# Kernel tuning notes

Measured on AMD Instinct MI355X. Metric: run time of the kernel, lower is better.

## Reference

```python
import jax, jax.numpy as jnp
import numpy as np

B, NQ, ISIZE = 8, 2048, 1024
H, D, NA = 8, 128, 8            # num_head, attn_dim, num_anchor
AH = H * D                      # ahsize = 1024
ASZ = NA * D                    # anchor_size = 1024
FH = 4096                       # _fhsize
ISZ_NET = FH * H // NA          # 4096, input dim of self.net
EPS = 1e-6


def setup_inputs() -> dict:
    key = jax.random.key(0)
    ks = jax.random.split(key, 12)
    def u(k, shape, fan_in):
        s = 1.0 / np.sqrt(fan_in)
        return jax.random.uniform(k, shape, jnp.float32, -s, s)
    return {
        "inputs": jax.random.normal(ks[0], (B, NQ, ISIZE), jnp.float32),
        "ln_g": jnp.ones((ISIZE,), jnp.float32),
        "ln_b": jnp.zeros((ISIZE,), jnp.float32),
        "q_anchor": u(ks[1], (H, NA, D), D),
        "W_qkv": u(ks[2], (ISIZE, 3 * AH), ISIZE), "b_qkv": jnp.zeros((3 * AH,), jnp.float32),
        "W_an": u(ks[3], (ASZ, FH), ASZ), "b_an": jnp.zeros((FH,), jnp.float32),
        "W_n1": u(ks[4], (ISZ_NET, AH), ISZ_NET), "b_n1": jnp.zeros((AH,), jnp.float32),
        "W_n2": u(ks[5], (AH, FH), AH), "b_n2": jnp.zeros((FH,), jnp.float32),
        "W_n3": u(ks[6], (FH, AH), FH), "b_n3": jnp.zeros((AH,), jnp.float32),
        "W_k": u(ks[7], (AH, AH), AH), "b_k": jnp.zeros((AH,), jnp.float32),
        "W_o": u(ks[8], (AH, ISIZE), AH), "b_o": jnp.zeros((ISIZE,), jnp.float32),
    }


def reference(inputs, ln_g, ln_b, q_anchor, W_qkv, b_qkv, W_an, b_an,
              W_n1, b_n1, W_n2, b_n2, W_n3, b_n3, W_k, b_k, W_o, b_o):
    b, nq = inputs.shape[:2]
    scale = 1.0 / np.sqrt(D)
    # pre-LayerNorm
    mu = jnp.mean(inputs, -1, keepdims=True)
    var = jnp.mean(jnp.square(inputs - mu), -1, keepdims=True)
    x = (inputs - mu) * jax.lax.rsqrt(var + EPS) * ln_g + ln_b
    # QKV projection
    qkv = (x @ W_qkv + b_qkv).reshape(b, nq, 3, H, D)
    q = jnp.transpose(qkv[:, :, 0], (0, 2, 1, 3))   # [b,H,nq,D]
    k = qkv[:, :, 1]                                  # [b,nq,H,D]
    v = qkv[:, :, 2]                                  # [b,nq,H,D]
    # stage 1: fixed anchors attend over the sequence
    sc1 = jax.nn.softmax(jnp.einsum('had,bnhd->bhan', q_anchor, k) * scale, axis=-1)
    out = jnp.einsum('bhan,bnhd->bhad', sc1, v).reshape(b, H, ASZ)   # [b,H,NA*D]
    # anchor_net (share_head Linear + ReLU)
    out = jax.nn.relu(out @ W_an + b_an)                              # [b,H,FH]
    # regroup head-major -> anchor-major
    out = out.reshape(b, H, NA, FH // NA).transpose(0, 2, 1, 3).reshape(b, NA, ISZ_NET)
    # net: bottleneck Linear -> Linear -> ReLU -> Linear
    out = jax.nn.relu((out @ W_n1 + b_n1) @ W_n2 + b_n2) @ W_n3 + b_n3  # [b,NA,AH]
    # stage 2: queries attend over anchors
    kk = (out @ W_k + b_k).reshape(b, NA, H, D)
    sc2 = jax.nn.softmax(jnp.einsum('bhqd,bahd->bhqa', q, kk) * scale, axis=-1)
    ov = out.reshape(b, NA, H, D)
    y = jnp.einsum('bhqa,bahd->bqhd', sc2, ov).reshape(b, nq, AH)
    return y @ W_o + b_o + inputs
```

## Files before the change

### kernel.cpp

```cpp
#include <hip/hip_runtime.h>
#include <cstdint>
#include <cstddef>

typedef unsigned short u16;
typedef __attribute__((ext_vector_type(8))) short short8;
typedef __attribute__((ext_vector_type(4))) float floatx4;
typedef __attribute__((ext_vector_type(16))) float floatx16;

__device__ __forceinline__ u16 f2bf(float f) {
  unsigned u = __float_as_uint(f);
  u += 0x7fffu + ((u >> 16) & 1u);
  return (u16)(u >> 16);
}
__device__ __forceinline__ float bf2f(u16 s) {
  return __uint_as_float(((unsigned)s) << 16);
}

__global__ __launch_bounds__(256) void ln_kernel(const float* __restrict__ x,
                                                 const float* __restrict__ g,
                                                 const float* __restrict__ bta,
                                                 u16* __restrict__ out) {
  const int row = blockIdx.x;
  const int tid = threadIdx.x;
  const float4 v = ((const float4*)(x + (size_t)row * 1024))[tid];
  float s = v.x + v.y + v.z + v.w;
#pragma unroll
  for (int o = 32; o > 0; o >>= 1) s += __shfl_down(s, o);
  __shared__ float red[4], red2[4];
  const int wv = tid >> 6, ln = tid & 63;
  if (ln == 0) red[wv] = s;
  __syncthreads();
  const float mean = (red[0] + red[1] + red[2] + red[3]) * (1.0f / 1024.0f);
  const float dx = v.x - mean, dy = v.y - mean, dz = v.z - mean, dw = v.w - mean;
  float s2 = dx * dx + dy * dy + dz * dz + dw * dw;
#pragma unroll
  for (int o = 32; o > 0; o >>= 1) s2 += __shfl_down(s2, o);
  if (ln == 0) red2[wv] = s2;
  __syncthreads();
  const float var = (red2[0] + red2[1] + red2[2] + red2[3]) * (1.0f / 1024.0f);
  const float rstd = rsqrtf(var + 1e-6f);
  const float4 gg = ((const float4*)g)[tid];
  const float4 bb = ((const float4*)bta)[tid];
  ushort4 o4;
  o4.x = f2bf(dx * rstd * gg.x + bb.x);
  o4.y = f2bf(dy * rstd * gg.y + bb.y);
  o4.z = f2bf(dz * rstd * gg.z + bb.z);
  o4.w = f2bf(dw * rstd * gg.w + bb.w);
  ((ushort4*)(out + (size_t)row * 1024))[tid] = o4;
}

__global__ __launch_bounds__(256) void transpose_bf16(const float* __restrict__ W,
                                                      u16* __restrict__ WT,
                                                      int K, int N) {
  __shared__ float t[32][33];
  const int kb = blockIdx.x * 32, nb = blockIdx.y * 32;
  const int tx = threadIdx.x & 31, ty = threadIdx.x >> 5;
#pragma unroll
  for (int i = ty; i < 32; i += 8) t[i][tx] = W[(size_t)(kb + i) * N + nb + tx];
  __syncthreads();
#pragma unroll
  for (int i = ty; i < 32; i += 8) WT[(size_t)(nb + i) * K + kb + tx] = f2bf(t[tx][i]);
}


__device__ __forceinline__ void stageG(const u16* __restrict__ gp, u16* lp, int K) {
  __builtin_amdgcn_global_load_lds((const __attribute__((address_space(1))) void*)gp,
                                   (__attribute__((address_space(3))) void*)lp, 16, 0, 0);
  __builtin_amdgcn_global_load_lds((const __attribute__((address_space(1))) void*)(gp + ((size_t)K << 6)),
                                   (__attribute__((address_space(3))) void*)(lp + 4096), 16, 0, 0);
}

__device__ __forceinline__ void rdA(short8 (&af)[2][4], const u16* sbuf, const int (&ab)[4],
                                    int halfoff) {
#pragma unroll
  for (int mi = 0; mi < 2; ++mi)
#pragma unroll
    for (int ks = 0; ks < 4; ++ks)
      af[mi][ks] = *(const short8*)(sbuf + halfoff + mi * 2048 + (ab[ks] ^ (mi << 5)));
}
__device__ __forceinline__ void rdB(short8 (&bf)[4], const u16* sbuf, const int (&bb)[4],
                                    int halfoff) {
#pragma unroll
  for (int ks = 0; ks < 4; ++ks)
    bf[ks] = *(const short8*)(sbuf + halfoff + bb[ks]);
}

template <int Q>
__device__ __forceinline__ void mfmaQ(floatx16 (&acc)[4][2], const short8 (&af)[2][4],
                                      const short8 (&bf)[4]) {
#pragma unroll
  for (int ks = 0; ks < 4; ++ks)
#pragma unroll
    for (int mi = 0; mi < 2; ++mi)
      acc[Q][mi] = __builtin_amdgcn_mfma_f32_32x32x16_bf16(af[mi][ks], bf[ks], acc[Q][mi], 0, 0, 0);
}

template <int B_>
__device__ __forceinline__ void gtile(int t, int NT, int K,
                                      u16 (&sA)[2][16384], u16 (&sB)[2][16384],
                                      const u16* gA_lo, const u16* gA_hi,
                                      const u16* gB_lo, const u16* gB_hi,
                                      u16* ldsA_cur, u16* ldsA_alt,
                                      u16* ldsB_cur, u16* ldsB_alt,
                                      const int (&ab)[4], const int (&bb)[4],
                                      floatx16 (&acc)[4][2],
                                      short8 (&afA)[2][4], short8 (&bfP)[4], short8 (&bfN)[4]) {
  rdA(afA, sA[B_], ab, 0);
  __builtin_amdgcn_sched_barrier(0);
  if (t + 1 < NT) stageG(gA_hi + ((t + 1) << 6), ldsA_alt + 8192, K);
  rdB(bfN, sB[B_], bb, 8192);
  asm volatile("s_waitcnt lgkmcnt(4)" ::: "memory");
  __builtin_amdgcn_sched_barrier(0);
  __builtin_amdgcn_s_setprio(1);
  mfmaQ<0>(acc, afA, bfP);
  __builtin_amdgcn_s_setprio(0);
  if (t + 1 < NT) stageG(gB_lo + ((t + 1) << 6), ldsB_alt, K);
  asm volatile("s_waitcnt lgkmcnt(0)" ::: "memory");
  __builtin_amdgcn_sched_barrier(0);
  __builtin_amdgcn_s_setprio(1);
  mfmaQ<1>(acc, afA, bfN);
  __builtin_amdgcn_s_setprio(0);
  rdA(afA, sA[B_], ab, 8192);
  __builtin_amdgcn_s_barrier();
  if (t + 2 < NT) stageG(gA_lo + ((t + 2) << 6), ldsA_cur, K);
  asm volatile("s_waitcnt lgkmcnt(0)" ::: "memory");
  __builtin_amdgcn_sched_barrier(0);
  __builtin_amdgcn_s_setprio(1);
  mfmaQ<2>(acc, afA, bfN);
  __builtin_amdgcn_s_setprio(0);
  if (t + 2 < NT) stageG(gB_hi + ((t + 2) << 6), ldsB_cur + 8192, K);
  if (t + 2 < NT) {
    asm volatile("s_waitcnt vmcnt(4)" ::: "memory");
  } else {
    asm volatile("s_waitcnt vmcnt(0)" ::: "memory");
  }
  __builtin_amdgcn_s_barrier();
  if (t + 1 < NT) rdB(bfN, sB[B_ ^ 1], bb, 0);
  __builtin_amdgcn_sched_barrier(0);
  __builtin_amdgcn_s_setprio(1);
  mfmaQ<3>(acc, afA, bfP);
  __builtin_amdgcn_s_setprio(0);
}

template <int EPI>
__global__ __launch_bounds__(512, 2) void gemm_bf16(const u16* __restrict__ A,
                                                    const u16* __restrict__ BT,
                                                    const float* __restrict__ bias,
                                                    const float* __restrict__ extra,
                                                    u16* __restrict__ outB,
                                                    float* __restrict__ outF,
                                                    int M, int N, int K) {
  __shared__ u16 sA[2][16384];
  __shared__ u16 sB[2][16384];
  const int tid = threadIdx.x;
  const int wave = tid >> 6, lane = tid & 63;
  const int m0 = blockIdx.x * 256, n0 = blockIdx.y * 256;
  const int wr = wave >> 2, wc = wave & 3;
  const int l31 = lane & 31, l5 = lane >> 5, l7 = lane & 7;
  const int NT = K >> 6;

  const int fa = l7 ^ (l31 >> 3);
  const int fb = l7 ^ ((wc * 4 + (l31 >> 3)) & 7);
  int ab[4], bb[4];
#pragma unroll
  for (int ks = 0; ks < 4; ++ks) {
    const int kg = (ks << 1) + l5;
    ab[ks] = (wr * 64 + l31) * 64 + (((kg ^ fa) & 7) << 3);
    bb[ks] = (wc * 32 + l31) * 64 + (((kg ^ fb) & 7) << 3);
  }
  const int srow = wave * 8 + (lane >> 3);
  const int scol = ((lane & 7) ^ (lane >> 3) ^ wave) << 3;
  const u16* gA_lo = A + (size_t)(m0 + srow) * K + scol;
  const u16* gA_hi = A + (size_t)(m0 + 128 + srow) * K + scol;
  const u16* gB_lo = BT + (size_t)(n0 + srow) * K + scol;
  const u16* gB_hi = BT + (size_t)(n0 + 128 + srow) * K + scol;

  floatx16 acc[4][2];
#pragma unroll
  for (int q = 0; q < 4; ++q)
#pragma unroll
    for (int mi = 0; mi < 2; ++mi)
#pragma unroll
      for (int r = 0; r < 16; ++r) acc[q][mi][r] = 0.f;

  stageG(gA_lo, &sA[0][0] + wave * 512, K);
  stageG(gA_hi, &sA[0][8192] + wave * 512, K);
  stageG(gB_lo, &sB[0][0] + wave * 512, K);
  stageG(gB_hi, &sB[0][8192] + wave * 512, K);
  stageG(gA_lo + 64, &sA[1][0] + wave * 512, K);
  stageG(gB_hi + 64, &sB[1][8192] + wave * 512, K);
  asm volatile("s_waitcnt vmcnt(4)" ::: "memory");
  __builtin_amdgcn_s_barrier();

  short8 afA[2][4], bfX[4], bfY[4];
  rdB(bfX, sB[0], bb, 0);
  __builtin_amdgcn_sched_barrier(0);

  for (int t = 0; t < NT; t += 2) {
    gtile<0>(t, NT, K, sA, sB, gA_lo, gA_hi, gB_lo, gB_hi,
             &sA[0][0] + wave * 512, &sA[1][0] + wave * 512,
             &sB[0][0] + wave * 512, &sB[1][0] + wave * 512, ab, bb, acc, afA, bfX, bfY);
    gtile<1>(t + 1, NT, K, sA, sB, gA_lo, gA_hi, gB_lo, gB_hi,
             &sA[1][0] + wave * 512, &sA[0][0] + wave * 512,
             &sB[1][0] + wave * 512, &sB[0][0] + wave * 512, ab, bb, acc, afA, bfY, bfX);
  }

#pragma unroll
  for (int q = 0; q < 4; ++q) {
    const int QM = q >> 1, QN = QM ^ (q & 1);
    const int n = n0 + QN * 128 + wc * 32 + l31;
    const float bs = bias[n];
#pragma unroll
    for (int mi = 0; mi < 2; ++mi) {
      const int mb = m0 + QM * 128 + wr * 64 + mi * 32 + 4 * l5;
#pragma unroll
      for (int reg = 0; reg < 16; ++reg) {
        const int m = mb + (reg & 3) + 8 * (reg >> 2);
        const float v = acc[q][mi][reg] + bs;
        if (EPI == 0)
          outB[(size_t)m * N + n] = f2bf(v);
        else
          outF[(size_t)m * N + n] = v + extra[(size_t)m * N + n];
      }
    }
  }
}

__global__ __launch_bounds__(256) void attn1_scores(const u16* __restrict__ qkv,
                                                    const float* __restrict__ q_anchor,
                                                    float* __restrict__ S) {
  __shared__ float qa[8][128];
  const int tid = threadIdx.x;
  const int chunk = blockIdx.x & 7, bh = blockIdx.x >> 3;
  const int b = bh >> 3, h = bh & 7;
  for (int i = tid; i < 1024; i += 256) qa[i >> 7][i & 127] = q_anchor[h * 1024 + i];
  __syncthreads();
  const float scale = 0.0883883476483184f;
  const int n = chunk * 256 + tid;
  const u16* kp = qkv + (size_t)(b * 2048 + n) * 3072 + 1024 + h * 128;
  float dots[8] = {0, 0, 0, 0, 0, 0, 0, 0};
#pragma unroll 8
  for (int dd = 0; dd < 128; dd += 4) {
    const ushort4 k4 = *(const ushort4*)(kp + dd);
    const float k0 = bf2f(k4.x), k1 = bf2f(k4.y), k2 = bf2f(k4.z), k3 = bf2f(k4.w);
#pragma unroll
    for (int a = 0; a < 8; ++a) {
      const float4 q4 = *(const float4*)&qa[a][dd];
      dots[a] += q4.x * k0 + q4.y * k1 + q4.z * k2 + q4.w * k3;
    }
  }
#pragma unroll
  for (int a = 0; a < 8; ++a) S[((size_t)(bh * 8 + a)) * 2048 + n] = dots[a] * scale;
}

__global__ __launch_bounds__(256) void attn1_softmax(float* __restrict__ S) {
  const int row = blockIdx.x;
  const int tid = threadIdx.x;
  float* Sp = S + (size_t)row * 2048;
  float4 v0 = ((const float4*)Sp)[tid * 2];
  float4 v1 = ((const float4*)Sp)[tid * 2 + 1];
  float mx = fmaxf(fmaxf(fmaxf(v0.x, v0.y), fmaxf(v0.z, v0.w)),
                   fmaxf(fmaxf(v1.x, v1.y), fmaxf(v1.z, v1.w)));
#pragma unroll
  for (int o = 32; o > 0; o >>= 1) mx = fmaxf(mx, __shfl_xor(mx, o));
  __shared__ float red[4];
  const int wv = tid >> 6, ln = tid & 63;
  if (ln == 0) red[wv] = mx;
  __syncthreads();
  mx = fmaxf(fmaxf(red[0], red[1]), fmaxf(red[2], red[3]));
  v0.x = __expf(v0.x - mx); v0.y = __expf(v0.y - mx);
  v0.z = __expf(v0.z - mx); v0.w = __expf(v0.w - mx);
  v1.x = __expf(v1.x - mx); v1.y = __expf(v1.y - mx);
  v1.z = __expf(v1.z - mx); v1.w = __expf(v1.w - mx);
  float sum = v0.x + v0.y + v0.z + v0.w + v1.x + v1.y + v1.z + v1.w;
#pragma unroll
  for (int o = 32; o > 0; o >>= 1) sum += __shfl_xor(sum, o);
  __shared__ float red2[4];
  if (ln == 0) red2[wv] = sum;
  __syncthreads();
  const float inv = 1.f / (red2[0] + red2[1] + red2[2] + red2[3]);
  v0.x *= inv; v0.y *= inv; v0.z *= inv; v0.w *= inv;
  v1.x *= inv; v1.y *= inv; v1.z *= inv; v1.w *= inv;
  ((float4*)Sp)[tid * 2] = v0;
  ((float4*)Sp)[tid * 2 + 1] = v1;
}

__global__ __launch_bounds__(256) void attn1_pv(const u16* __restrict__ qkv,
                                                const float* __restrict__ S,
                                                float* __restrict__ pvpart) {
  __shared__ float P[8][256];
  const int tid = threadIdx.x;
  const int chunk = blockIdx.x & 7, bh = blockIdx.x >> 3;
  const int b = bh >> 3, h = bh & 7;
  for (int i = tid; i < 2048; i += 256) {
    const int a = i >> 8, n = i & 255;
    P[a][n] = S[((size_t)(bh * 8 + a)) * 2048 + chunk * 256 + n];
  }
  __syncthreads();
  const int d = tid & 127, half = tid >> 7;
  const int nbase = chunk * 256 + half * 128;
  const u16* vp = qkv + (size_t)(b * 2048 + nbase) * 3072 + 2048 + h * 128 + d;
  float acc[8] = {0.f};
  for (int n = 0; n < 128; n += 4) {
    const float v0 = bf2f(vp[(size_t)n * 3072]);
    const float v1 = bf2f(vp[(size_t)(n + 1) * 3072]);
    const float v2 = bf2f(vp[(size_t)(n + 2) * 3072]);
    const float v3 = bf2f(vp[(size_t)(n + 3) * 3072]);
#pragma unroll
    for (int a = 0; a < 8; ++a) {
      const float4 s4 = *(const float4*)&P[a][half * 128 + n];
      acc[a] += s4.x * v0 + s4.y * v1 + s4.z * v2 + s4.w * v3;
    }
  }
  const int split = chunk * 2 + half;
#pragma unroll
  for (int a = 0; a < 8; ++a)
    pvpart[((size_t)split * 64 + bh) * 1024 + a * 128 + d] = acc[a];
}

__global__ __launch_bounds__(256) void mlp_mfma(const float* __restrict__ A,
                                                const float* __restrict__ W,
                                                float* __restrict__ part,
                                                int K, int N, int KC) {
  __shared__ float sW[64][33];
  const int tid = threadIdx.x;
  const int lane = tid & 63, wave = tid >> 6;
  const int wm = wave * 16;
  const int n0 = blockIdx.x * 64;
  const int kbeg = blockIdx.y * KC;
  const int l15 = lane & 15, kq8 = (lane >> 4) * 8;
  const int arow = wm + l15;

  floatx4 acc[4];
  const floatx4 zero = {0.f, 0.f, 0.f, 0.f};
#pragma unroll
  for (int j = 0; j < 4; ++j) acc[j] = zero;

  for (int kc = 0; kc < KC; kc += 32) {
    const int kbase = kbeg + kc;
    __syncthreads();
#pragma unroll
    for (int p = 0; p < 8; ++p) {
      const int k = p * 4 + wave;
      sW[lane][k] = W[(size_t)(kbase + k) * N + n0 + lane];
    }
    const float* ap = A + (size_t)arow * K + kbase + kq8;
    const float4 a0 = *(const float4*)ap;
    const float4 a1 = *(const float4*)(ap + 4);
    short8 af;
    af[0] = (short)f2bf(a0.x); af[1] = (short)f2bf(a0.y);
    af[2] = (short)f2bf(a0.z); af[3] = (short)f2bf(a0.w);
    af[4] = (short)f2bf(a1.x); af[5] = (short)f2bf(a1.y);
    af[6] = (short)f2bf(a1.z); af[7] = (short)f2bf(a1.w);
    __syncthreads();
#pragma unroll
    for (int j = 0; j < 4; ++j) {
      const float* wp = &sW[j * 16 + l15][kq8];
      short8 bf;
      bf[0] = (short)f2bf(wp[0]); bf[1] = (short)f2bf(wp[1]);
      bf[2] = (short)f2bf(wp[2]); bf[3] = (short)f2bf(wp[3]);
      bf[4] = (short)f2bf(wp[4]); bf[5] = (short)f2bf(wp[5]);
      bf[6] = (short)f2bf(wp[6]); bf[7] = (short)f2bf(wp[7]);
      acc[j] = __builtin_amdgcn_mfma_f32_16x16x32_bf16(af, bf, acc[j], 0, 0, 0);
    }
  }
  const int q = lane >> 4;
#pragma unroll
  for (int j = 0; j < 4; ++j)
#pragma unroll
    for (int r = 0; r < 4; ++r) {
      const int m = wm + q * 4 + r;
      const int n = n0 + j * 16 + l15;
      part[((size_t)blockIdx.y * 64 + m) * N + n] = acc[j][r];
    }
}

__global__ __launch_bounds__(256) void mlp_reduce(const float* __restrict__ part,
                                                  const float* __restrict__ bias,
                                                  float* __restrict__ out,
                                                  int N, int nsplit, int relu, int perm) {
  const int idx = blockIdx.x * 256 + threadIdx.x;
  const int e = idx * 4;
  if (e >= 64 * N) return;
  const int row = e / N, col = e - row * N;
  float4 acc;
  if (bias) acc = *(const float4*)&bias[col];
  else { acc.x = 0.f; acc.y = 0.f; acc.z = 0.f; acc.w = 0.f; }
  for (int s = 0; s < nsplit; ++s) {
    const float4 p = *(const float4*)&part[((size_t)s * 64 + row) * N + col];
    acc.x += p.x; acc.y += p.y; acc.z += p.z; acc.w += p.w;
  }
  if (relu) {
    acc.x = fmaxf(acc.x, 0.f); acc.y = fmaxf(acc.y, 0.f);
    acc.z = fmaxf(acc.z, 0.f); acc.w = fmaxf(acc.w, 0.f);
  }
  size_t oidx;
  if (!perm) {
    oidx = (size_t)row * N + col;
  } else {
    const int b = row >> 3, h = row & 7;
    oidx = (size_t)(b * 8 + (col >> 9)) * 4096 + h * 512 + (col & 511);
  }
  *(float4*)&out[oidx] = acc;
}

__global__ __launch_bounds__(256) void attn2_kernel(const u16* __restrict__ qkv,
                                                    const float* __restrict__ kk,
                                                    const float* __restrict__ onet,
                                                    u16* __restrict__ y) {
  __shared__ float kkl[8][128];
  __shared__ float ovl[8][128];
  const int tid = threadIdx.x;
  const int chunk = blockIdx.x & 7, bh = blockIdx.x >> 3;
  const int b = bh >> 3, h = bh & 7;
  for (int i = tid; i < 1024; i += 256) {
    const int a = i >> 7, d = i & 127;
    kkl[a][d] = kk[(size_t)(b * 8 + a) * 1024 + h * 128 + d];
    ovl[a][d] = onet[(size_t)(b * 8 + a) * 1024 + h * 128 + d];
  }
  __syncthreads();
  const int n = chunk * 256 + tid;
  const u16* qp = qkv + (size_t)(b * 2048 + n) * 3072 + h * 128;
  float dots[8] = {0, 0, 0, 0, 0, 0, 0, 0};
#pragma unroll 4
  for (int dd = 0; dd < 128; dd += 4) {
    const ushort4 q4 = *(const ushort4*)(qp + dd);
    const float q0 = bf2f(q4.x), q1 = bf2f(q4.y), q2 = bf2f(q4.z), q3 = bf2f(q4.w);
#pragma unroll
    for (int a = 0; a < 8; ++a) {
      const float4 k4 = *(const float4*)&kkl[a][dd];
      dots[a] += k4.x * q0 + k4.y * q1 + k4.z * q2 + k4.w * q3;
    }
  }
  const float scale = 0.0883883476483184f;
  float mx = -1e30f;
#pragma unroll
  for (int a = 0; a < 8; ++a) {
    dots[a] *= scale;
    mx = fmaxf(mx, dots[a]);
  }
  float p[8];
  float sum = 0.f;
#pragma unroll
  for (int a = 0; a < 8; ++a) {
    p[a] = __expf(dots[a] - mx);
    sum += p[a];
  }
  const float inv = 1.f / sum;
#pragma unroll
  for (int a = 0; a < 8; ++a) p[a] *= inv;
  u16* yp = y + (size_t)(b * 2048 + n) * 1024 + h * 128;
#pragma unroll 4
  for (int dd = 0; dd < 128; dd += 4) {
    float a0 = 0, a1 = 0, a2 = 0, a3 = 0;
#pragma unroll
    for (int a = 0; a < 8; ++a) {
      const float4 o4 = *(const float4*)&ovl[a][dd];
      a0 += p[a] * o4.x;
      a1 += p[a] * o4.y;
      a2 += p[a] * o4.z;
      a3 += p[a] * o4.w;
    }
    ushort4 o;
    o.x = f2bf(a0);
    o.y = f2bf(a1);
    o.z = f2bf(a2);
    o.w = f2bf(a3);
    *(ushort4*)(yp + dd) = o;
  }
}

extern "C" void kernel_launch(void* const* d_in, const int* in_sizes, int n_in,
                              void* d_out, int out_size, void* d_ws, size_t ws_size,
                              hipStream_t stream) {
  const float* inputs = (const float*)d_in[0];
  const float* ln_g = (const float*)d_in[1];
  const float* ln_b = (const float*)d_in[2];
  const float* q_anchor = (const float*)d_in[3];
  const float* W_qkv = (const float*)d_in[4];
  const float* b_qkv = (const float*)d_in[5];
  const float* W_an = (const float*)d_in[6];
  const float* b_an = (const float*)d_in[7];
  const float* W_n1 = (const float*)d_in[8];
  const float* b_n1 = (const float*)d_in[9];
  const float* W_n2 = (const float*)d_in[10];
  const float* b_n2 = (const float*)d_in[11];
  const float* W_n3 = (const float*)d_in[12];
  const float* b_n3 = (const float*)d_in[13];
  const float* W_k = (const float*)d_in[14];
  const float* b_k = (const float*)d_in[15];
  const float* W_o = (const float*)d_in[16];
  const float* b_o = (const float*)d_in[17];
  float* out = (float*)d_out;

  char* ws = (char*)d_ws;
  u16* qkv = (u16*)(ws);
  u16* xbf = (u16*)(ws + 100663296);
  float* S = (float*)(ws + 100663296);
  float* part = (float*)(ws + 109051904);
  u16* WqkvT = (u16*)(ws + 134217728);
  u16* WoT = (u16*)(ws + 140509184);
  float* att1 = (float*)(ws + 142606336);
  float* anp = (float*)(ws + 142868480);
  float* h1 = (float*)(ws + 143917056);
  float* h2 = (float*)(ws + 144179200);
  float* onet = (float*)(ws + 145227776);
  float* kkb = (float*)(ws + 145489920);

  ln_kernel<<<16384, 256, 0, stream>>>(inputs, ln_g, ln_b, xbf);
  transpose_bf16<<<dim3(32, 96), 256, 0, stream>>>(W_qkv, WqkvT, 1024, 3072);
  transpose_bf16<<<dim3(32, 32), 256, 0, stream>>>(W_o, WoT, 1024, 1024);
  gemm_bf16<0><<<dim3(64, 12), 512, 0, stream>>>(xbf, WqkvT, b_qkv, nullptr, qkv, nullptr,
                                                 16384, 3072, 1024);
  attn1_scores<<<512, 256, 0, stream>>>(qkv, q_anchor, S);
  attn1_softmax<<<512, 256, 0, stream>>>(S);
  attn1_pv<<<512, 256, 0, stream>>>(qkv, S, part);
  mlp_reduce<<<64, 256, 0, stream>>>(part, nullptr, att1, 1024, 16, 0, 0);
  mlp_mfma<<<dim3(64, 8), 256, 0, stream>>>(att1, W_an, part, 1024, 4096, 128);
  mlp_reduce<<<256, 256, 0, stream>>>(part, b_an, anp, 4096, 8, 1, 1);
  mlp_mfma<<<dim3(16, 32), 256, 0, stream>>>(anp, W_n1, part, 4096, 1024, 128);
  mlp_reduce<<<64, 256, 0, stream>>>(part, b_n1, h1, 1024, 32, 0, 0);
  mlp_mfma<<<dim3(64, 8), 256, 0, stream>>>(h1, W_n2, part, 1024, 4096, 128);
  mlp_reduce<<<256, 256, 0, stream>>>(part, b_n2, h2, 4096, 8, 1, 0);
  mlp_mfma<<<dim3(16, 32), 256, 0, stream>>>(h2, W_n3, part, 4096, 1024, 128);
  mlp_reduce<<<64, 256, 0, stream>>>(part, b_n3, onet, 1024, 32, 0, 0);
  mlp_mfma<<<dim3(16, 16), 256, 0, stream>>>(onet, W_k, part, 1024, 1024, 64);
  mlp_reduce<<<64, 256, 0, stream>>>(part, b_k, kkb, 1024, 16, 0, 0);
  attn2_kernel<<<512, 256, 0, stream>>>(qkv, kkb, onet, xbf);
  gemm_bf16<1><<<dim3(64, 4), 512, 0, stream>>>(xbf, WoT, b_o, inputs, nullptr, out,
                                                16384, 1024, 1024);
}
```

Measured before the change: 587.1 us.

## Replace split-K partial buffers and reduce kernels with atomic accumulation into bias-initialized outputs

Removes the separate mlp_reduce launches. The split-K MLP GEMMs and the attention-1 PV kernel now atomically add into output buffers that a single init kernel pre-fills with biases or zeros. ReLU and the head-to-anchor permutation move into the A-operand load of the next GEMM, and the two weight transposes are merged into one launch. This saves about six launches and the partial-buffer write and read traffic, but adds fp32 atomics, nondeterministic summation order, and fewer split-K blocks (larger KC).

```diff
diff --git a/kernel.cpp b/kernel.cpp
--- a/kernel.cpp
+++ b/kernel.cpp
@@ -49,17 +49,56 @@
   ((ushort4*)(out + (size_t)row * 1024))[tid] = o4;
 }
 
-__global__ __launch_bounds__(256) void transpose_bf16(const float* __restrict__ W,
-                                                      u16* __restrict__ WT,
-                                                      int K, int N) {
+__global__ __launch_bounds__(256) void transpose2_bf16(const float* __restrict__ Wq,
+                                                       u16* __restrict__ WqT,
+                                                       const float* __restrict__ Wo,
+                                                       u16* __restrict__ WoT) {
   __shared__ float t[32][33];
-  const int kb = blockIdx.x * 32, nb = blockIdx.y * 32;
+  const float* W;
+  u16* WT;
+  int N, yb;
+  if (blockIdx.y < 96) { W = Wq; WT = WqT; N = 3072; yb = blockIdx.y; }
+  else { W = Wo; WT = WoT; N = 1024; yb = blockIdx.y - 96; }
+  const int kb = blockIdx.x * 32, nb = yb * 32;
   const int tx = threadIdx.x & 31, ty = threadIdx.x >> 5;
 #pragma unroll
   for (int i = ty; i < 32; i += 8) t[i][tx] = W[(size_t)(kb + i) * N + nb + tx];
   __syncthreads();
 #pragma unroll
-  for (int i = ty; i < 32; i += 8) WT[(size_t)(nb + i) * K + kb + tx] = f2bf(t[tx][i]);
+  for (int i = ty; i < 32; i += 8) WT[(size_t)(nb + i) * 1024 + kb + tx] = f2bf(t[tx][i]);
+}
+
+__global__ __launch_bounds__(256) void init_bufs(const float* __restrict__ b_an,
+                                                 const float* __restrict__ b_n1,
+                                                 const float* __restrict__ b_n2,
+                                                 const float* __restrict__ b_n3,
+                                                 const float* __restrict__ b_k,
+                                                 float* __restrict__ att1,
+                                                 float* __restrict__ anp,
+                                                 float* __restrict__ h1,
+                                                 float* __restrict__ h2,
+                                                 float* __restrict__ onet,
+                                                 float* __restrict__ kkb) {
+  const int i = blockIdx.x * 256 + threadIdx.x;
+  if (i < 16384) {
+    float4 z; z.x = 0.f; z.y = 0.f; z.z = 0.f; z.w = 0.f;
+    ((float4*)att1)[i] = z;
+  } else if (i < 81920) {
+    const int j = i - 16384;
+    ((float4*)anp)[j] = ((const float4*)b_an)[j & 1023];
+  } else if (i < 98304) {
+    const int j = i - 81920;
+    ((float4*)h1)[j] = ((const float4*)b_n1)[j & 255];
+  } else if (i < 163840) {
+    const int j = i - 98304;
+    ((float4*)h2)[j] = ((const float4*)b_n2)[j & 1023];
+  } else if (i < 180224) {
+    const int j = i - 163840;
+    ((float4*)onet)[j] = ((const float4*)b_n3)[j & 255];
+  } else {
+    const int j = i - 180224;
+    ((float4*)kkb)[j] = ((const float4*)b_k)[j & 255];
+  }
 }
 
 
@@ -287,7 +326,7 @@
 
 __global__ __launch_bounds__(256) void attn1_pv(const u16* __restrict__ qkv,
                                                 const float* __restrict__ S,
-                                                float* __restrict__ pvpart) {
+                                                float* __restrict__ att1) {
   __shared__ float P[8][256];
   const int tid = threadIdx.x;
   const int chunk = blockIdx.x & 7, bh = blockIdx.x >> 3;
@@ -312,15 +351,15 @@
       acc[a] += s4.x * v0 + s4.y * v1 + s4.z * v2 + s4.w * v3;
     }
   }
-  const int split = chunk * 2 + half;
 #pragma unroll
   for (int a = 0; a < 8; ++a)
-    pvpart[((size_t)split * 64 + bh) * 1024 + a * 128 + d] = acc[a];
-}
-
+    atomicAdd(&att1[(size_t)bh * 1024 + a * 128 + d], acc[a]);
+}
+
+template <int AMODE>
 __global__ __launch_bounds__(256) void mlp_mfma(const float* __restrict__ A,
                                                 const float* __restrict__ W,
-                                                float* __restrict__ part,
+                                                float* __restrict__ outp,
                                                 int K, int N, int KC) {
   __shared__ float sW[64][33];
   const int tid = threadIdx.x;
@@ -344,9 +383,21 @@
       const int k = p * 4 + wave;
       sW[lane][k] = W[(size_t)(kbase + k) * N + n0 + lane];
     }
-    const float* ap = A + (size_t)arow * K + kbase + kq8;
-    const float4 a0 = *(const float4*)ap;
-    const float4 a1 = *(const float4*)(ap + 4);
+    const float* ap;
+    if (AMODE == 2) {
+      const int k = kbase + kq8;
+      ap = A + (size_t)(arow >> 3) * 32768 + (size_t)(k >> 9) * 4096 + (arow & 7) * 512 + (k & 511);
+    } else {
+      ap = A + (size_t)arow * K + kbase + kq8;
+    }
+    float4 a0 = *(const float4*)ap;
+    float4 a1 = *(const float4*)(ap + 4);
+    if (AMODE >= 1) {
+      a0.x = fmaxf(a0.x, 0.f); a0.y = fmaxf(a0.y, 0.f);
+      a0.z = fmaxf(a0.z, 0.f); a0.w = fmaxf(a0.w, 0.f);
+      a1.x = fmaxf(a1.x, 0.f); a1.y = fmaxf(a1.y, 0.f);
+      a1.z = fmaxf(a1.z, 0.f); a1.w = fmaxf(a1.w, 0.f);
+    }
     short8 af;
     af[0] = (short)f2bf(a0.x); af[1] = (short)f2bf(a0.y);
     af[2] = (short)f2bf(a0.z); af[3] = (short)f2bf(a0.w);
@@ -371,37 +422,8 @@
     for (int r = 0; r < 4; ++r) {
       const int m = wm + q * 4 + r;
       const int n = n0 + j * 16 + l15;
-      part[((size_t)blockIdx.y * 64 + m) * N + n] = acc[j][r];
-    }
-}
-
-__global__ __launch_bounds__(256) void mlp_reduce(const float* __restrict__ part,
-                                                  const float* __restrict__ bias,
-                                                  float* __restrict__ out,
-                                                  int N, int nsplit, int relu, int perm) {
-  const int idx = blockIdx.x * 256 + threadIdx.x;
-  const int e = idx * 4;
-  if (e >= 64 * N) return;
-  const int row = e / N, col = e - row * N;
-  float4 acc;
-  if (bias) acc = *(const float4*)&bias[col];
-  else { acc.x = 0.f; acc.y = 0.f; acc.z = 0.f; acc.w = 0.f; }
-  for (int s = 0; s < nsplit; ++s) {
-    const float4 p = *(const float4*)&part[((size_t)s * 64 + row) * N + col];
-    acc.x += p.x; acc.y += p.y; acc.z += p.z; acc.w += p.w;
-  }
-  if (relu) {
-    acc.x = fmaxf(acc.x, 0.f); acc.y = fmaxf(acc.y, 0.f);
-    acc.z = fmaxf(acc.z, 0.f); acc.w = fmaxf(acc.w, 0.f);
-  }
-  size_t oidx;
-  if (!perm) {
-    oidx = (size_t)row * N + col;
-  } else {
-    const int b = row >> 3, h = row & 7;
-    oidx = (size_t)(b * 8 + (col >> 9)) * 4096 + h * 512 + (col & 511);
-  }
-  *(float4*)&out[oidx] = acc;
+      atomicAdd(&outp[(size_t)m * N + n], acc[j][r]);
+    }
 }
 
 __global__ __launch_bounds__(256) void attn2_kernel(const u16* __restrict__ qkv,
@@ -497,7 +519,6 @@
   u16* qkv = (u16*)(ws);
   u16* xbf = (u16*)(ws + 100663296);
   float* S = (float*)(ws + 100663296);
-  float* part = (float*)(ws + 109051904);
   u16* WqkvT = (u16*)(ws + 134217728);
   u16* WoT = (u16*)(ws + 140509184);
   float* att1 = (float*)(ws + 142606336);
@@ -508,24 +529,19 @@
   float* kkb = (float*)(ws + 145489920);
 
   ln_kernel<<<16384, 256, 0, stream>>>(inputs, ln_g, ln_b, xbf);
-  transpose_bf16<<<dim3(32, 96), 256, 0, stream>>>(W_qkv, WqkvT, 1024, 3072);
-  transpose_bf16<<<dim3(32, 32), 256, 0, stream>>>(W_o, WoT, 1024, 1024);
+  transpose2_bf16<<<dim3(32, 128), 256, 0, stream>>>(W_qkv, WqkvT, W_o, WoT);
+  init_bufs<<<768, 256, 0, stream>>>(b_an, b_n1, b_n2, b_n3, b_k,
+                                     att1, anp, h1, h2, onet, kkb);
   gemm_bf16<0><<<dim3(64, 12), 512, 0, stream>>>(xbf, WqkvT, b_qkv, nullptr, qkv, nullptr,
                                                  16384, 3072, 1024);
   attn1_scores<<<512, 256, 0, stream>>>(qkv, q_anchor, S);
   attn1_softmax<<<512, 256, 0, stream>>>(S);
-  attn1_pv<<<512, 256, 0, stream>>>(qkv, S, part);
-  mlp_reduce<<<64, 256, 0, stream>>>(part, nullptr, att1, 1024, 16, 0, 0);
-  mlp_mfma<<<dim3(64, 8), 256, 0, stream>>>(att1, W_an, part, 1024, 4096, 128);
-  mlp_reduce<<<256, 256, 0, stream>>>(part, b_an, anp, 4096, 8, 1, 1);
-  mlp_mfma<<<dim3(16, 32), 256, 0, stream>>>(anp, W_n1, part, 4096, 1024, 128);
-  mlp_reduce<<<64, 256, 0, stream>>>(part, b_n1, h1, 1024, 32, 0, 0);
-  mlp_mfma<<<dim3(64, 8), 256, 0, stream>>>(h1, W_n2, part, 1024, 4096, 128);
-  mlp_reduce<<<256, 256, 0, stream>>>(part, b_n2, h2, 4096, 8, 1, 0);
-  mlp_mfma<<<dim3(16, 32), 256, 0, stream>>>(h2, W_n3, part, 4096, 1024, 128);
-  mlp_reduce<<<64, 256, 0, stream>>>(part, b_n3, onet, 1024, 32, 0, 0);
-  mlp_mfma<<<dim3(16, 16), 256, 0, stream>>>(onet, W_k, part, 1024, 1024, 64);
-  mlp_reduce<<<64, 256, 0, stream>>>(part, b_k, kkb, 1024, 16, 0, 0);
+  attn1_pv<<<512, 256, 0, stream>>>(qkv, S, att1);
+  mlp_mfma<0><<<dim3(64, 4), 256, 0, stream>>>(att1, W_an, anp, 1024, 4096, 256);
+  mlp_mfma<2><<<dim3(16, 16), 256, 0, stream>>>(anp, W_n1, h1, 4096, 1024, 256);
+  mlp_mfma<0><<<dim3(64, 4), 256, 0, stream>>>(h1, W_n2, h2, 1024, 4096, 256);
+  mlp_mfma<1><<<dim3(16, 16), 256, 0, stream>>>(h2, W_n3, onet, 4096, 1024, 256);
+  mlp_mfma<0><<<dim3(16, 8), 256, 0, stream>>>(onet, W_k, kkb, 1024, 1024, 128);
   attn2_kernel<<<512, 256, 0, stream>>>(qkv, kkb, onet, xbf);
   gemm_bf16<1><<<dim3(64, 4), 512, 0, stream>>>(xbf, WoT, b_o, inputs, nullptr, out,
                                                 16384, 1024, 1024);
```

Measured after the change: 578.1 us. No clear change (-1.5%).
